# Kernel optimization log

Hardware: AMD Instinct MI355X
Metric: run time of the kernel (lower is better)

Reference implementation:

```python
import jax, jax.numpy as jnp
import numpy as np

B, N_NODE, E_PER, C, HID, HEADS, IN, NL = 16, 1024, 8192, 16, 128, 4, 32, 2
N = B * N_NODE
NEG_SLOPE = 0.2


def setup_inputs() -> dict:
    key = jax.random.key(0)
    ks = jax.random.split(key, 16)
    obs = jax.random.normal(ks[0], (N, IN), jnp.float32)
    # per-graph random edges, guaranteed no self-loops (GATv2Conv re-adds them once)
    src_l = jax.random.randint(ks[1], (B, E_PER), 0, N_NODE)
    off = jax.random.randint(ks[2], (B, E_PER), 1, N_NODE)
    dst_l = (src_l + off) % N_NODE
    base = (jnp.arange(B) * N_NODE)[:, None]
    edge_index = jnp.stack([(src_l + base).reshape(-1), (dst_l + base).reshape(-1)]).astype(jnp.int32)

    def lin(k, fi, fo):
        return (jax.random.normal(k, (fi, fo), jnp.float32) / np.sqrt(fi)).astype(jnp.float32)

    def gat(k):
        sk = jax.random.split(k, 3)
        return {
            'Wl': (jax.random.normal(sk[0], (NL, HID, HEADS * HID), jnp.float32) / np.sqrt(HID)),
            'bl': jnp.zeros((NL, HEADS * HID), jnp.float32),
            'Wr': (jax.random.normal(sk[1], (NL, HID, HEADS * HID), jnp.float32) / np.sqrt(HID)),
            'br': jnp.zeros((NL, HEADS * HID), jnp.float32),
            'att': (jax.random.normal(sk[2], (NL, HEADS, HID), jnp.float32) / np.sqrt(HID)),
            'bias': jnp.zeros((NL, HID), jnp.float32),
            'g': jnp.ones((NL, HID), jnp.float32),
            'beta': jnp.zeros((NL, HID), jnp.float32),
        }

    inp = {'obs': obs, 'edge_index': edge_index, 'n_node': N_NODE,
           'emb_W': lin(ks[3], IN, HID), 'emb_b': jnp.zeros((HID,), jnp.float32),
           'pool_W': lin(ks[4], HID, C), 'pool_b': jnp.zeros((C,), jnp.float32),
           'mlp_W1': lin(ks[5], HID, 4 * HID), 'mlp_b1': jnp.zeros((4 * HID,), jnp.float32),
           'mlp_W2': lin(ks[6], 4 * HID, HID), 'mlp_b2': jnp.zeros((HID,), jnp.float32)}
    for nm, d in (('low', gat(ks[7])), ('high', gat(ks[8]))):
        for k2, v in d.items():
            inp[nm + '_' + k2] = v
    return inp


def _layer_norm(x, g, b):
    mu = x.mean(-1, keepdims=True)
    v = jnp.mean((x - mu) ** 2, -1, keepdims=True)
    return (x - mu) / jnp.sqrt(v + 1e-5) * g + b


def _gatv2(x, src, dst, Wl, bl, Wr, br, att, bias):
    # GATv2Conv: heads H, concat=False (mean over heads), eval mode (no dropout)
    n = x.shape[0]
    H, D = att.shape
    xl = (x @ Wl + bl).reshape(n, H, D)  # source transform (lin_l)
    xr = (x @ Wr + br).reshape(n, H, D)  # target transform (lin_r)
    e = jax.nn.leaky_relu(xl[src] + xr[dst], NEG_SLOPE)  # [E,H,D]
    logit = jnp.einsum('ehd,hd->eh', e, att)
    m = jax.ops.segment_max(logit, dst, num_segments=n)
    p = jnp.exp(logit - m[dst])
    z = jax.ops.segment_sum(p, dst, num_segments=n)
    alpha = p / z[dst]
    out = jax.ops.segment_sum(alpha[:, :, None] * xl[src], dst, num_segments=n)
    return out.mean(axis=1) + bias


def _gat_stack(h, src, dst, Wl, bl, Wr, br, att, bias, g, beta):
    h_res = h
    nl = Wl.shape[0]
    for j in range(nl):
        h_in = h
        h = _gatv2(h, src, dst, Wl[j], bl[j], Wr[j], br[j], att[j], bias[j])
        h = _layer_norm(h, g[j], beta[j])
        if j != nl - 1:
            h = jax.nn.silu(h)
        h = h + h_in  # use_res=True
    return h + h_res


def _forward(obs, edge_index, n_node, emb_W, emb_b, pool_W, pool_b, mlp_W1, mlp_b1, mlp_W2, mlp_b2,
             low_Wl, low_bl, low_Wr, low_br, low_att, low_bias, low_g, low_beta,
             high_Wl, high_bl, high_Wr, high_br, high_att, high_bias, high_g, high_beta):
    n = obs.shape[0]
    h = obs @ emb_W + emb_b
    hh = h
    # low-level edges + self-loops (GATv2Conv add_self_loops; input has none)
    loops = jnp.arange(n, dtype=edge_index.dtype)
    src = jnp.concatenate([edge_index[0], loops])
    dst = jnp.concatenate([edge_index[1], loops])
    h = _gat_stack(h, src, dst, low_Wl, low_bl, low_Wr, low_br, low_att, low_bias, low_g, low_beta)
    # soft pooling
    pooling = jax.nn.softmax(h @ pool_W + pool_b, axis=-1)  # dim=1 == last dim on 2D
    b = n // n_node
    c = pooling.shape[-1]
    s = pooling.reshape(b, n_node, c)
    count = jnp.maximum(s.sum(axis=1), 1e-5)  # sT @ ones, clamp_min(1e-5)
    Hf = jnp.einsum('bnc,bnd->bcd', s, h.reshape(b, n_node, -1)) / count[:, :, None]
    Hf = Hf.reshape(b * c, -1)
    # high-level: fully connected per-graph cluster edges (self-loops already present once)
    hr = jnp.repeat(jnp.arange(c, dtype=jnp.int32), c)
    hc = jnp.tile(jnp.arange(c, dtype=jnp.int32), c)
    offb = (jnp.arange(b, dtype=jnp.int32) * c)[:, None]
    hsrc = (hr[None, :] + offb).reshape(-1)
    hdst = (hc[None, :] + offb).reshape(-1)
    Hf = _gat_stack(Hf, hsrc, hdst, high_Wl, high_bl, high_Wr, high_br, high_att, high_bias, high_g, high_beta)
    # unpool + residual MLP (BaseMLP flat=True: hidden=4*HID, Tanh, residual)
    l_H = jnp.einsum('bnc,bcd->bnd', s, Hf.reshape(b, c, -1)).reshape(n, -1)
    x = l_H + hh
    return jnp.tanh(x @ mlp_W1 + mlp_b1) @ mlp_W2 + mlp_b2 + x


def reference(obs, edge_index, n_node, emb_W, emb_b, pool_W, pool_b, mlp_W1, mlp_b1, mlp_W2, mlp_b2,
              low_Wl, low_bl, low_Wr, low_br, low_att, low_bias, low_g, low_beta,
              high_Wl, high_bl, high_Wr, high_br, high_att, high_bias, high_g, high_beta):
    return _forward(obs, edge_index, n_node, emb_W, emb_b, pool_W, pool_b, mlp_W1, mlp_b1, mlp_W2, mlp_b2,
                    low_Wl, low_bl, low_Wr, low_br, low_att, low_bias, low_g, low_beta,
                    high_Wl, high_bl, high_Wr, high_br, high_att, high_bias, high_g, high_beta)
```

## Files before the change

kernel.cpp:

```cpp
#include <hip/hip_runtime.h>
#include <math.h>

#define NTOT  16384
#define NNODE 1024

typedef unsigned short u16;
typedef unsigned short u16x8 __attribute__((ext_vector_type(8)));
typedef short s16x8 __attribute__((ext_vector_type(8)));
typedef float f32x4 __attribute__((ext_vector_type(4)));

static __device__ __forceinline__ float b2f(u16 u) {
  return __uint_as_float(((unsigned)u) << 16);
}
static __device__ __forceinline__ u16 f2b(float f) {
  unsigned x = __float_as_uint(f);
  return (u16)((x + 0x7FFFu + ((x >> 16) & 1u)) >> 16);
}

__global__ __launch_bounds__(64) void emb_k(const float* __restrict__ obs,
    const float* __restrict__ W, const float* __restrict__ b,
    float* __restrict__ h, float* __restrict__ hh, u16* __restrict__ h_bf)
{
  int n = blockIdx.x, l = threadIdx.x;
  __shared__ float ob[32];
  if (l < 32) ob[l] = obs[n * 32 + l];
  __syncthreads();
  float a0 = b[l], a1 = b[64 + l];
  #pragma unroll
  for (int k = 0; k < 32; ++k) {
    float o = ob[k];
    a0 = fmaf(o, W[k * 128 + l], a0);
    a1 = fmaf(o, W[k * 128 + 64 + l], a1);
  }
  size_t base = (size_t)n * 128;
  h[base + l] = a0;  h[base + 64 + l] = a1;
  hh[base + l] = a0; hh[base + 64 + l] = a1;
  h_bf[base + l] = f2b(a0); h_bf[base + 64 + l] = f2b(a1);
}

__global__ void hist_k(const int* __restrict__ ei, int E0, int* __restrict__ deg)
{
  int i = blockIdx.x * blockDim.x + threadIdx.x;
  int ET = E0 + NTOT;
  if (i < ET) {
    int d = (i < E0) ? ei[E0 + i] : (i - E0);
    atomicAdd(&deg[d], 1);
  }
}

__global__ __launch_bounds__(256) void scan_k(const int* __restrict__ deg,
    int* __restrict__ off, int* __restrict__ cursor)
{
  __shared__ int part[256];
  int t = threadIdx.x;
  int base = t * 64;
  int sum = 0;
  for (int i = 0; i < 64; ++i) sum += deg[base + i];
  part[t] = sum;
  __syncthreads();
  if (t == 0) {
    int run = 0;
    for (int i = 0; i < 256; ++i) { int v = part[i]; part[i] = run; run += v; }
  }
  __syncthreads();
  int run = part[t];
  for (int i = 0; i < 64; ++i) {
    off[base + i] = run; cursor[base + i] = run;
    run += deg[base + i];
  }
  if (t == 255) off[NTOT] = run;
}

__global__ void scat_k(const int* __restrict__ ei, int E0,
    int* __restrict__ cursor, int* __restrict__ csr_src)
{
  int i = blockIdx.x * blockDim.x + threadIdx.x;
  int ET = E0 + NTOT;
  if (i < ET) {
    int s, d;
    if (i < E0) { s = ei[i]; d = ei[E0 + i]; } else { s = d = i - E0; }
    int pos = atomicAdd(&cursor[d], 1);
    csr_src[pos] = s;
  }
}

__global__ void hi_k(int* __restrict__ hi_off, int* __restrict__ hi_src)
{
  int t = threadIdx.x;
  hi_off[t] = t * 16;
  if (t == 0) hi_off[256] = 4096;
  for (int i = t; i < 4096; i += 256) {
    int u = i >> 4;
    hi_src[i] = (u & ~15) + (i & 15);
  }
}

__global__ void wq_k(const float* __restrict__ W, u16* __restrict__ out,
                     int K, int N, int total)
{
  int idx = blockIdx.x * 256 + threadIdx.x;
  if (idx >= total) return;
  int kn = K * N;
  int m = idx / kn, r = idx - m * kn;
  int n = r / K, k = r - n * K;
  out[idx] = f2b(W[(size_t)m * kn + (size_t)k * N + n]);
}

__global__ __launch_bounds__(256) void gemm_bf16(
    const u16* __restrict__ A, const u16* __restrict__ Bt,
    const float* __restrict__ bias,
    float* __restrict__ Cf, u16* __restrict__ Cb,
    const float* __restrict__ res,
    int M, int K, int N, int act)
{
  __shared__ u16 Al[128][128];
  __shared__ u16 Bl[128][128];
  const int tid = threadIdx.x;
  const int bm = blockIdx.x * 128, bn = blockIdx.y * 128;
  const int w = tid >> 6, l = tid & 63;
  const int fr = l & 15;
  const int kg = l >> 4;
  const int sr = tid >> 1;
  const int sh = (tid & 1) << 3;

  f32x4 acc[2][8];
  #pragma unroll
  for (int a = 0; a < 2; ++a)
    #pragma unroll
    for (int b = 0; b < 8; ++b)
      acc[a][b] = (f32x4){0.f, 0.f, 0.f, 0.f};

  for (int k0 = 0; k0 < K; k0 += 128) {
    __syncthreads();
    const u16* As = A + (size_t)(bm + sr) * K + k0 + (sh << 3);
    const u16* Bs = Bt + (size_t)(bn + sr) * K + k0 + (sh << 3);
    #pragma unroll
    for (int i = 0; i < 8; ++i) {
      int gs = (sh + i) ^ (sr & 7);
      *(uint4*)&Al[sr][gs << 3] = *(const uint4*)(As + (i << 3));
    }
    #pragma unroll
    for (int i = 0; i < 8; ++i) {
      int gs = (sh + i) ^ (sr & 7);
      *(uint4*)&Bl[sr][gs << 3] = *(const uint4*)(Bs + (i << 3));
    }
    __syncthreads();
    #pragma unroll
    for (int ks = 0; ks < 4; ++ks) {
      const int g = (ks << 2) + kg;
      const int ar0 = w * 32 + fr, ar1 = ar0 + 16;
      s16x8 a0 = *(const s16x8*)&Al[ar0][(g ^ (ar0 & 7)) << 3];
      s16x8 a1 = *(const s16x8*)&Al[ar1][(g ^ (ar1 & 7)) << 3];
      #pragma unroll
      for (int nr = 0; nr < 8; ++nr) {
        const int br = nr * 16 + fr;
        s16x8 bb = *(const s16x8*)&Bl[br][(g ^ (br & 7)) << 3];
        acc[0][nr] = __builtin_amdgcn_mfma_f32_16x16x32_bf16(a0, bb, acc[0][nr], 0, 0, 0);
        acc[1][nr] = __builtin_amdgcn_mfma_f32_16x16x32_bf16(a1, bb, acc[1][nr], 0, 0, 0);
      }
    }
  }

  #pragma unroll
  for (int mr = 0; mr < 2; ++mr) {
    const int row0 = bm + w * 32 + mr * 16 + (kg << 2);
    #pragma unroll
    for (int nr = 0; nr < 8; ++nr) {
      const int col = bn + nr * 16 + fr;
      const float bb = bias[col];
      #pragma unroll
      for (int j = 0; j < 4; ++j) {
        float v = acc[mr][nr][j] + bb;
        if (act) v = tanhf(v);
        size_t o = (size_t)(row0 + j) * N + col;
        if (res) v += res[o];
        if (Cf) Cf[o] = v;
        if (Cb) Cb[o] = f2b(v);
      }
    }
  }
}

__global__ __launch_bounds__(64) void gat_agg(
    const u16* __restrict__ xl, const u16* __restrict__ xr,
    const int* __restrict__ off, const int* __restrict__ srcs,
    const float* __restrict__ att, const float* __restrict__ bias,
    const float* __restrict__ g, const float* __restrict__ beta,
    float* __restrict__ h, u16* __restrict__ h_bf,
    const float* __restrict__ res2, int do_silu, int swz)
{
  int b = blockIdx.x, l = threadIdx.x;
  int dst;
  if (swz) {
    int xcd = b & 7, i = b >> 3;
    dst = (((xcd << 1) + (i >> 10)) << 10) | (i & 1023);
  } else dst = b;

  float xrr[8], attr[8];
  {
    u16x8 vx = *(const u16x8*)(xr + (size_t)dst * 512 + l * 8);
    #pragma unroll
    for (int i = 0; i < 8; ++i) xrr[i] = b2f(vx[i]);
    const float4 a0 = *(const float4*)(att + l * 8);
    const float4 a1 = *(const float4*)(att + l * 8 + 4);
    attr[0] = a0.x; attr[1] = a0.y; attr[2] = a0.z; attr[3] = a0.w;
    attr[4] = a1.x; attr[5] = a1.y; attr[6] = a1.z; attr[7] = a1.w;
  }
  int e0 = off[dst], e1 = off[dst + 1];
  float m = -1e30f, z = 0.f;
  float acc[8] = {0.f, 0.f, 0.f, 0.f, 0.f, 0.f, 0.f, 0.f};
  for (int e = e0; e < e1; ++e) {
    u16x8 vv = *(const u16x8*)(xl + (size_t)srcs[e] * 512 + l * 8);
    float xv[8];
    #pragma unroll
    for (int i = 0; i < 8; ++i) xv[i] = b2f(vv[i]);
    float part = 0.f;
    #pragma unroll
    for (int i = 0; i < 8; ++i) {
      float v = xv[i] + xrr[i];
      v = v > 0.f ? v : 0.2f * v;
      part = fmaf(v, attr[i], part);
    }
    part += __shfl_xor(part, 1); part += __shfl_xor(part, 2);
    part += __shfl_xor(part, 4); part += __shfl_xor(part, 8);
    float mn = fmaxf(m, part);
    float s = __expf(m - mn);
    float p = __expf(part - mn);
    z = z * s + p;
    #pragma unroll
    for (int i = 0; i < 8; ++i) acc[i] = fmaf(acc[i], s, p * xv[i]);
    m = mn;
  }
  float inv = 0.25f / z;
  int d0 = (l & 15) * 8;
  float o[8];
  #pragma unroll
  for (int i = 0; i < 8; ++i) {
    float v = acc[i] * inv;
    v += __shfl_xor(v, 16);
    v += __shfl_xor(v, 32);
    o[i] = v + bias[d0 + i];
  }
  float ssum = 0.f;
  #pragma unroll
  for (int i = 0; i < 8; ++i) ssum += o[i];
  ssum += __shfl_xor(ssum, 1); ssum += __shfl_xor(ssum, 2);
  ssum += __shfl_xor(ssum, 4); ssum += __shfl_xor(ssum, 8);
  float mu = ssum * (1.f / 128.f);
  float vs = 0.f;
  #pragma unroll
  for (int i = 0; i < 8; ++i) { float d = o[i] - mu; vs += d * d; }
  vs += __shfl_xor(vs, 1); vs += __shfl_xor(vs, 2);
  vs += __shfl_xor(vs, 4); vs += __shfl_xor(vs, 8);
  float rstd = rsqrtf(vs * (1.f / 128.f) + 1e-5f);
  if (l < 16) {
    size_t base = (size_t)dst * 128 + d0;
    float out[8];
    u16x8 hb;
    #pragma unroll
    for (int i = 0; i < 8; ++i) {
      float y = (o[i] - mu) * rstd * g[d0 + i] + beta[d0 + i];
      if (do_silu) y = y / (1.f + __expf(-y));
      float r = h[base + i];
      if (res2) r += res2[base + i];
      out[i] = y + r;
      hb[i] = f2b(out[i]);
    }
    *(float4*)(h + base) = make_float4(out[0], out[1], out[2], out[3]);
    *(float4*)(h + base + 4) = make_float4(out[4], out[5], out[6], out[7]);
    *(u16x8*)(h_bf + base) = hb;
  }
}

__global__ __launch_bounds__(256) void pool_k(const float* __restrict__ h,
    const float* __restrict__ W, const float* __restrict__ b, float* __restrict__ s)
{
  __shared__ float hs[16 * 130];
  __shared__ float Ws[128 * 16];
  int t = threadIdx.x;
  int n0 = blockIdx.x * 16;
  #pragma unroll
  for (int i = 0; i < 8; ++i) {
    int idx = t + 256 * i;
    hs[(idx >> 7) * 130 + (idx & 127)] = h[(size_t)n0 * 128 + idx];
    Ws[idx] = W[idx];
  }
  __syncthreads();
  int nl = t >> 4, c = t & 15;
  float acc = b[c];
  for (int k = 0; k < 128; ++k) acc = fmaf(hs[nl * 130 + k], Ws[k * 16 + c], acc);
  float mx = acc;
  mx = fmaxf(mx, __shfl_xor(mx, 1)); mx = fmaxf(mx, __shfl_xor(mx, 2));
  mx = fmaxf(mx, __shfl_xor(mx, 4)); mx = fmaxf(mx, __shfl_xor(mx, 8));
  float p = __expf(acc - mx), sum = p;
  sum += __shfl_xor(sum, 1); sum += __shfl_xor(sum, 2);
  sum += __shfl_xor(sum, 4); sum += __shfl_xor(sum, 8);
  s[(size_t)(n0 + nl) * 16 + c] = p / sum;
}

__global__ __launch_bounds__(128) void hf_k(const float* __restrict__ s,
    const float* __restrict__ h, float* __restrict__ Hf, float* __restrict__ HfRes,
    u16* __restrict__ Hf_bf)
{
  int b = blockIdx.x >> 4, c = blockIdx.x & 15, d = threadIdx.x;
  float acc = 0.f, cnt = 0.f;
  for (int n = 0; n < NNODE; ++n) {
    float sv = s[(size_t)(b * NNODE + n) * 16 + c];
    cnt += sv;
    acc = fmaf(sv, h[(size_t)(b * NNODE + n) * 128 + d], acc);
  }
  cnt = fmaxf(cnt, 1e-5f);
  float v = acc / cnt;
  size_t o = (size_t)(b * 16 + c) * 128 + d;
  Hf[o] = v; HfRes[o] = v; Hf_bf[o] = f2b(v);
}

__global__ __launch_bounds__(64) void unpool_k(const float* __restrict__ s,
    const float* __restrict__ Hf, const float* __restrict__ hh,
    float* __restrict__ x, u16* __restrict__ x_bf)
{
  int n = blockIdx.x, l = threadIdx.x;
  int b = n >> 10;
  float a0 = 0.f, a1 = 0.f;
  #pragma unroll
  for (int c = 0; c < 16; ++c) {
    float sv = s[(size_t)n * 16 + c];
    const float* hp = Hf + (size_t)((b << 4) + c) * 128;
    a0 = fmaf(sv, hp[l], a0);
    a1 = fmaf(sv, hp[64 + l], a1);
  }
  size_t base = (size_t)n * 128;
  float v0 = a0 + hh[base + l], v1 = a1 + hh[base + 64 + l];
  x[base + l] = v0; x[base + 64 + l] = v1;
  x_bf[base + l] = f2b(v0); x_bf[base + 64 + l] = f2b(v1);
}

extern "C" void kernel_launch(void* const* d_in, const int* in_sizes, int n_in,
                              void* d_out, int out_size, void* d_ws, size_t ws_size,
                              hipStream_t stream) {
  (void)n_in; (void)out_size; (void)ws_size;
  const float* obs    = (const float*)d_in[0];
  const int*   ei     = (const int*)d_in[1];
  const float* emb_W  = (const float*)d_in[3];
  const float* emb_b  = (const float*)d_in[4];
  const float* pool_W = (const float*)d_in[5];
  const float* pool_b = (const float*)d_in[6];
  const float* mlp_W1 = (const float*)d_in[7];
  const float* mlp_b1 = (const float*)d_in[8];
  const float* mlp_W2 = (const float*)d_in[9];
  const float* mlp_b2 = (const float*)d_in[10];
  const float* lWl = (const float*)d_in[11]; const float* lbl = (const float*)d_in[12];
  const float* lWr = (const float*)d_in[13]; const float* lbr = (const float*)d_in[14];
  const float* latt = (const float*)d_in[15]; const float* lbias = (const float*)d_in[16];
  const float* lg = (const float*)d_in[17]; const float* lbeta = (const float*)d_in[18];
  const float* hWl = (const float*)d_in[19]; const float* hbl = (const float*)d_in[20];
  const float* hWr = (const float*)d_in[21]; const float* hbr = (const float*)d_in[22];
  const float* hatt = (const float*)d_in[23]; const float* hbias = (const float*)d_in[24];
  const float* hg = (const float*)d_in[25]; const float* hbeta = (const float*)d_in[26];

  const int E0 = in_sizes[1] / 2;
  const int ET = E0 + NTOT;

  char* p = (char*)d_ws;
  auto alloc = [&](size_t bytes) -> void* {
    void* q = (void*)p;
    p += (bytes + 255) & ~(size_t)255;
    return q;
  };
  float* h      = (float*)alloc((size_t)NTOT * 128 * 4);
  float* hh     = (float*)alloc((size_t)NTOT * 128 * 4);
  u16*   h_bf   = (u16*)alloc((size_t)NTOT * 128 * 2);
  u16*   xl_bf  = (u16*)alloc((size_t)NTOT * 512 * 2);
  u16*   xr_bf  = (u16*)alloc((size_t)NTOT * 512 * 2);
  u16*   x_bf   = (u16*)alloc((size_t)NTOT * 128 * 2);
  float* s      = (float*)alloc((size_t)NTOT * 16 * 4);
  float* Hf     = (float*)alloc(256 * 128 * 4);
  float* HfRes  = (float*)alloc(256 * 128 * 4);
  u16*   Hf_bf  = (u16*)alloc(256 * 128 * 2);
  u16*   hxl    = (u16*)alloc(256 * 512 * 2);
  u16*   hxr    = (u16*)alloc(256 * 512 * 2);
  u16*   lWlT   = (u16*)alloc(2 * 512 * 128 * 2);
  u16*   lWrT   = (u16*)alloc(2 * 512 * 128 * 2);
  u16*   hWlT   = (u16*)alloc(2 * 512 * 128 * 2);
  u16*   hWrT   = (u16*)alloc(2 * 512 * 128 * 2);
  u16*   W1T    = (u16*)alloc(512 * 128 * 2);
  u16*   W2T    = (u16*)alloc(128 * 512 * 2);
  int* deg      = (int*)alloc((size_t)NTOT * 4);
  int* off      = (int*)alloc((size_t)(NTOT + 1) * 4);
  int* cursor   = (int*)alloc((size_t)NTOT * 4);
  int* csr      = (int*)alloc((size_t)ET * 4);
  int* hi_off   = (int*)alloc(257 * 4);
  int* hi_src   = (int*)alloc(4096 * 4);
  u16* t_bf     = xl_bf;

  wq_k<<<(2 * 65536 + 255) / 256, 256, 0, stream>>>(lWl, lWlT, 128, 512, 2 * 65536);
  wq_k<<<(2 * 65536 + 255) / 256, 256, 0, stream>>>(lWr, lWrT, 128, 512, 2 * 65536);
  wq_k<<<(2 * 65536 + 255) / 256, 256, 0, stream>>>(hWl, hWlT, 128, 512, 2 * 65536);
  wq_k<<<(2 * 65536 + 255) / 256, 256, 0, stream>>>(hWr, hWrT, 128, 512, 2 * 65536);
  wq_k<<<(65536 + 255) / 256, 256, 0, stream>>>(mlp_W1, W1T, 128, 512, 65536);
  wq_k<<<(65536 + 255) / 256, 256, 0, stream>>>(mlp_W2, W2T, 512, 128, 65536);

  hipMemsetAsync(deg, 0, (size_t)NTOT * 4, stream);
  emb_k<<<NTOT, 64, 0, stream>>>(obs, emb_W, emb_b, h, hh, h_bf);
  hist_k<<<(ET + 255) / 256, 256, 0, stream>>>(ei, E0, deg);
  scan_k<<<1, 256, 0, stream>>>(deg, off, cursor);
  scat_k<<<(ET + 255) / 256, 256, 0, stream>>>(ei, E0, cursor, csr);
  hi_k<<<1, 256, 0, stream>>>(hi_off, hi_src);

  for (int j = 0; j < 2; ++j) {
    gemm_bf16<<<dim3(NTOT / 128, 4), 256, 0, stream>>>(h_bf, lWlT + j * 65536,
        lbl + j * 512, nullptr, xl_bf, nullptr, NTOT, 128, 512, 0);
    gemm_bf16<<<dim3(NTOT / 128, 4), 256, 0, stream>>>(h_bf, lWrT + j * 65536,
        lbr + j * 512, nullptr, xr_bf, nullptr, NTOT, 128, 512, 0);
    gat_agg<<<NTOT, 64, 0, stream>>>(xl_bf, xr_bf, off, csr, latt + j * 512,
        lbias + j * 128, lg + j * 128, lbeta + j * 128, h, h_bf,
        j == 1 ? hh : nullptr, j == 0 ? 1 : 0, 1);
  }

  pool_k<<<NTOT / 16, 256, 0, stream>>>(h, pool_W, pool_b, s);
  hf_k<<<256, 128, 0, stream>>>(s, h, Hf, HfRes, Hf_bf);

  for (int j = 0; j < 2; ++j) {
    gemm_bf16<<<dim3(2, 4), 256, 0, stream>>>(Hf_bf, hWlT + j * 65536,
        hbl + j * 512, nullptr, hxl, nullptr, 256, 128, 512, 0);
    gemm_bf16<<<dim3(2, 4), 256, 0, stream>>>(Hf_bf, hWrT + j * 65536,
        hbr + j * 512, nullptr, hxr, nullptr, 256, 128, 512, 0);
    gat_agg<<<256, 64, 0, stream>>>(hxl, hxr, hi_off, hi_src, hatt + j * 512,
        hbias + j * 128, hg + j * 128, hbeta + j * 128, Hf, Hf_bf,
        j == 1 ? HfRes : nullptr, j == 0 ? 1 : 0, 0);
  }

  float* x = (float*)d_out;
  unpool_k<<<NTOT, 64, 0, stream>>>(s, Hf, hh, x, x_bf);
  gemm_bf16<<<dim3(NTOT / 128, 4), 256, 0, stream>>>(x_bf, W1T, mlp_b1,
      nullptr, t_bf, nullptr, NTOT, 128, 512, 1);
  gemm_bf16<<<dim3(NTOT / 128, 1), 256, 0, stream>>>(t_bf, W2T, mlp_b2,
      x, nullptr, x, NTOT, 512, 128, 0);
}
```

Before: 469.5 us.

## Split pooled-feature reduction into chunked partials and prefetch gather rows in GAT aggregation

The cluster-feature pooling kernel, which had each block walk all 1024 nodes serially, is replaced by a two-stage reduction. The first stage has 512 blocks each reduce a 32-node chunk through shared memory into partial sums and counts. The second stage sums the partials and writes Hf, HfRes and Hf_bf. Separately, the GAT edge loop now prefetches the next neighbour's source index and feature row one iteration ahead, to hide gather latency. The cost is a scratch buffer, an extra launch and extra registers in the aggregation kernel.

```diff
diff --git a/kernel.cpp b/kernel.cpp
--- a/kernel.cpp
+++ b/kernel.cpp
@@ -209,8 +209,14 @@
   int e0 = off[dst], e1 = off[dst + 1];
   float m = -1e30f, z = 0.f;
   float acc[8] = {0.f, 0.f, 0.f, 0.f, 0.f, 0.f, 0.f, 0.f};
+  int sB = (e0 + 1 < e1) ? srcs[e0 + 1] : 0;
+  u16x8 vcur = *(const u16x8*)(xl + (size_t)srcs[e0] * 512 + l * 8);
   for (int e = e0; e < e1; ++e) {
-    u16x8 vv = *(const u16x8*)(xl + (size_t)srcs[e] * 512 + l * 8);
+    u16x8 vv = vcur;
+    if (e + 1 < e1) {
+      vcur = *(const u16x8*)(xl + (size_t)sB * 512 + l * 8);
+      if (e + 2 < e1) sB = srcs[e + 2];
+    }
     float xv[8];
     #pragma unroll
     for (int i = 0; i < 8; ++i) xv[i] = b2f(vv[i]);
@@ -224,11 +230,11 @@
     part += __shfl_xor(part, 1); part += __shfl_xor(part, 2);
     part += __shfl_xor(part, 4); part += __shfl_xor(part, 8);
     float mn = fmaxf(m, part);
-    float s = __expf(m - mn);
+    float sc = __expf(m - mn);
     float p = __expf(part - mn);
-    z = z * s + p;
-    #pragma unroll
-    for (int i = 0; i < 8; ++i) acc[i] = fmaf(acc[i], s, p * xv[i]);
+    z = z * sc + p;
+    #pragma unroll
+    for (int i = 0; i < 8; ++i) acc[i] = fmaf(acc[i], sc, p * xv[i]);
     m = mn;
   }
   float inv = 0.25f / z;
@@ -298,20 +304,58 @@
   s[(size_t)(n0 + nl) * 16 + c] = p / sum;
 }
 
-__global__ __launch_bounds__(128) void hf_k(const float* __restrict__ s,
-    const float* __restrict__ h, float* __restrict__ Hf, float* __restrict__ HfRes,
-    u16* __restrict__ Hf_bf)
-{
-  int b = blockIdx.x >> 4, c = blockIdx.x & 15, d = threadIdx.x;
-  float acc = 0.f, cnt = 0.f;
-  for (int n = 0; n < NNODE; ++n) {
-    float sv = s[(size_t)(b * NNODE + n) * 16 + c];
-    cnt += sv;
-    acc = fmaf(sv, h[(size_t)(b * NNODE + n) * 128 + d], acc);
-  }
-  cnt = fmaxf(cnt, 1e-5f);
-  float v = acc / cnt;
-  size_t o = (size_t)(b * 16 + c) * 128 + d;
+#define HF_CHUNK 32
+#define HF_NCH   32
+__global__ __launch_bounds__(256) void hfp_k(const float* __restrict__ s,
+    const float* __restrict__ h, float* __restrict__ part, float* __restrict__ cpart)
+{
+  __shared__ float ss[HF_CHUNK][16];
+  __shared__ float hs[HF_CHUNK][128];
+  int b = blockIdx.x >> 5, chunk = blockIdx.x & 31;
+  int n0 = b * NNODE + chunk * HF_CHUNK;
+  int t = threadIdx.x;
+  if (t < 128) {
+    float4 v = *(const float4*)(s + (size_t)(n0 + (t >> 2)) * 16 + (t & 3) * 4);
+    *(float4*)&ss[t >> 2][(t & 3) * 4] = v;
+  }
+  #pragma unroll
+  for (int i = 0; i < 4; ++i) {
+    int idx = t + 256 * i;
+    int row = idx >> 5, c4 = (idx & 31) * 4;
+    *(float4*)&hs[row][c4] = *(const float4*)(h + (size_t)(n0 + row) * 128 + c4);
+  }
+  __syncthreads();
+  int d = t & 127, cg = (t >> 7) * 8;
+  float acc[8] = {};
+  for (int n = 0; n < HF_CHUNK; ++n) {
+    float hv = hs[n][d];
+    #pragma unroll
+    for (int i = 0; i < 8; ++i) acc[i] = fmaf(ss[n][cg + i], hv, acc[i]);
+  }
+  float* po = part + (size_t)chunk * 32768 + (size_t)(b * 16 + cg) * 128 + d;
+  #pragma unroll
+  for (int i = 0; i < 8; ++i) po[i * 128] = acc[i];
+  if (t < 16) {
+    float c = 0.f;
+    #pragma unroll
+    for (int n = 0; n < HF_CHUNK; ++n) c += ss[n][t];
+    cpart[chunk * 256 + b * 16 + t] = c;
+  }
+}
+
+__global__ __launch_bounds__(256) void hfr_k(const float* __restrict__ part,
+    const float* __restrict__ cpart, float* __restrict__ Hf,
+    float* __restrict__ HfRes, u16* __restrict__ Hf_bf)
+{
+  int o = blockIdx.x * 256 + threadIdx.x;
+  int bc = o >> 7;
+  float a = 0.f, cnt = 0.f;
+  #pragma unroll 8
+  for (int ch = 0; ch < HF_NCH; ++ch) {
+    a += part[(size_t)ch * 32768 + o];
+    cnt += cpart[ch * 256 + bc];
+  }
+  float v = a / fmaxf(cnt, 1e-5f);
   Hf[o] = v; HfRes[o] = v; Hf_bf[o] = f2b(v);
 }
 
@@ -379,6 +423,8 @@
   u16*   Hf_bf  = (u16*)alloc(256 * 128 * 2);
   u16*   hxl    = (u16*)alloc(256 * 512 * 2);
   u16*   hxr    = (u16*)alloc(256 * 512 * 2);
+  float* hfPart = (float*)alloc((size_t)HF_NCH * 32768 * 4);
+  float* hfCnt  = (float*)alloc((size_t)HF_NCH * 256 * 4);
   u16*   lWlT   = (u16*)alloc(2 * 512 * 128 * 2);
   u16*   lWrT   = (u16*)alloc(2 * 512 * 128 * 2);
   u16*   hWlT   = (u16*)alloc(2 * 512 * 128 * 2);
@@ -418,7 +464,8 @@
   }
 
   pool_k<<<NTOT / 16, 256, 0, stream>>>(h, pool_W, pool_b, s);
-  hf_k<<<256, 128, 0, stream>>>(s, h, Hf, HfRes, Hf_bf);
+  hfp_k<<<16 * HF_NCH, 256, 0, stream>>>(s, h, hfPart, hfCnt);
+  hfr_k<<<128, 256, 0, stream>>>(hfPart, hfCnt, Hf, HfRes, Hf_bf);
 
   for (int j = 0; j < 2; ++j) {
     gemm_bf16<<<dim3(2, 4), 256, 0, stream>>>(Hf_bf, hWlT + j * 65536,
```

Result: faster. 421.1 us (-10.3%).
